# Kernel tuning notes

Hardware: AMD Instinct MI355X
Metric: run time of the kernel (lower is better)

The kernel has to match this reference:

```python
import jax, jax.numpy as jnp
import numpy as np

N, D = 8192, 4096

def setup_inputs() -> dict:
    key = jax.random.key(0)
    k1, k2 = jax.random.split(key)
    # inputs = [mean | var]; shift uniform by +0.1 so var > 0 (log + division)
    inputs = jax.random.uniform(k1, (N, 2 * D), dtype=jnp.float32) + 0.1
    targets = jax.random.normal(k2, (N, D), dtype=jnp.float32)
    return {"inputs": inputs, "targets": targets}

def reference(inputs, targets):
    size = targets.shape[1]
    mean = inputs[:, :size]          # [N, D]
    var = inputs[:, size:]           # [N, D]
    diff = mean - targets            # [N, D]
    mid = diff / var                 # [N, D]
    lg = jnp.log(jnp.sum(var))
    # Faithful to the torch code: full DxD gram matrix, then its trace.
    out = jnp.trace(jnp.matmul(diff.T, mid)) + lg
    return out
```

## Files before the change

kernel.cpp:

```cpp
#include <hip/hip_runtime.h>


constexpr int N = 8192;
constexpr int D = 4096;
constexpr int BLOCKS = 2048;
constexpr int THREADS = 256;

__global__ __launch_bounds__(THREADS) void loss_partial_kernel(
    const float* __restrict__ inputs,
    const float* __restrict__ targets,
    float* __restrict__ partials)
{
    const long long total4  = (long long)N * D / 4;
    const long long nthread = (long long)gridDim.x * blockDim.x;

    float s1 = 0.0f;
    float s2 = 0.0f;

    long long i = (long long)blockIdx.x * blockDim.x + threadIdx.x;
    #pragma unroll 4
    for (int it = 0; it < 16; ++it, i += nthread) {
        const long long row  = i >> 10;
        const long long col4 = (i & 1023) << 2;

        const float4 m = *(const float4*)(inputs  + row * (2LL * D) + col4);
        const float4 v = *(const float4*)(inputs  + row * (2LL * D) + D + col4);
        const float4 t = *(const float4*)(targets + (i << 2));

        const float d0 = m.x - t.x;
        const float d1 = m.y - t.y;
        const float d2 = m.z - t.z;
        const float d3 = m.w - t.w;

        s1 += d0 * d0 * __builtin_amdgcn_rcpf(v.x);
        s1 += d1 * d1 * __builtin_amdgcn_rcpf(v.y);
        s1 += d2 * d2 * __builtin_amdgcn_rcpf(v.z);
        s1 += d3 * d3 * __builtin_amdgcn_rcpf(v.w);
        s2 += (v.x + v.y) + (v.z + v.w);
    }

    #pragma unroll
    for (int off = 32; off > 0; off >>= 1) {
        s1 += __shfl_down(s1, off, 64);
        s2 += __shfl_down(s2, off, 64);
    }

    __shared__ float l1[THREADS / 64];
    __shared__ float l2[THREADS / 64];
    const int wave = threadIdx.x >> 6;
    const int lane = threadIdx.x & 63;
    if (lane == 0) { l1[wave] = s1; l2[wave] = s2; }
    __syncthreads();

    if (threadIdx.x == 0) {
        float a = l1[0] + l1[1] + l1[2] + l1[3];
        float b = l2[0] + l2[1] + l2[2] + l2[3];
        partials[blockIdx.x]          = a;
        partials[BLOCKS + blockIdx.x] = b;
    }
}

__global__ __launch_bounds__(256) void loss_final_kernel(
    const float* __restrict__ partials,
    float* __restrict__ out)
{
    double s1 = 0.0, s2 = 0.0;
    for (int i = threadIdx.x; i < BLOCKS; i += 256) {
        s1 += (double)partials[i];
        s2 += (double)partials[BLOCKS + i];
    }

    #pragma unroll
    for (int off = 32; off > 0; off >>= 1) {
        s1 += __shfl_down(s1, off, 64);
        s2 += __shfl_down(s2, off, 64);
    }

    __shared__ double l1[4];
    __shared__ double l2[4];
    const int wave = threadIdx.x >> 6;
    const int lane = threadIdx.x & 63;
    if (lane == 0) { l1[wave] = s1; l2[wave] = s2; }
    __syncthreads();

    if (threadIdx.x == 0) {
        const double a = l1[0] + l1[1] + l1[2] + l1[3];
        const double b = l2[0] + l2[1] + l2[2] + l2[3];
        out[0] = (float)(a + log(b));
    }
}

extern "C" void kernel_launch(void* const* d_in, const int* in_sizes, int n_in,
                              void* d_out, int out_size, void* d_ws, size_t ws_size,
                              hipStream_t stream) {
    const float* inputs  = (const float*)d_in[0];
    const float* targets = (const float*)d_in[1];
    float* out      = (float*)d_out;
    float* partials = (float*)d_ws;

    loss_partial_kernel<<<BLOCKS, THREADS, 0, stream>>>(inputs, targets, partials);
    loss_final_kernel<<<1, 256, 0, stream>>>(partials, out);
}
```

Measured before the change: 80.15 us.

## Fuse final reduction into main kernel via atomics and last-block finalize

Drops the separate finalize kernel. Each block now atomically adds its partial sums into a workspace, and the last block (found with an atomic counter) writes the loss. The streaming loads switch to nontemporal loads with 32-bit index math and a smaller unroll, and the launch bounds gain an occupancy hint. In exchange a memset launch is added, and the float atomic accumulation is non-deterministic and less precise than the earlier double reduction.

New measurement: 262.8 us. 228% more time.

```diff
diff --git a/kernel.cpp b/kernel.cpp
--- a/kernel.cpp
+++ b/kernel.cpp
@@ -1,4 +1,5 @@
 #include <hip/hip_runtime.h>
+#include <math.h>
 
 
 constexpr int N = 8192;
@@ -6,26 +7,31 @@
 constexpr int BLOCKS = 2048;
 constexpr int THREADS = 256;
 
-__global__ __launch_bounds__(THREADS) void loss_partial_kernel(
+typedef float f32x4 __attribute__((ext_vector_type(4)));
+
+__global__ __launch_bounds__(THREADS, 8) void loss_fused_kernel(
     const float* __restrict__ inputs,
     const float* __restrict__ targets,
-    float* __restrict__ partials)
+    float* __restrict__ ws,
+    float* __restrict__ out)
 {
-    const long long total4  = (long long)N * D / 4;
-    const long long nthread = (long long)gridDim.x * blockDim.x;
+    constexpr unsigned NTHREAD = (unsigned)BLOCKS * THREADS;
 
     float s1 = 0.0f;
     float s2 = 0.0f;
 
-    long long i = (long long)blockIdx.x * blockDim.x + threadIdx.x;
-    #pragma unroll 4
-    for (int it = 0; it < 16; ++it, i += nthread) {
-        const long long row  = i >> 10;
-        const long long col4 = (i & 1023) << 2;
+    unsigned i = blockIdx.x * (unsigned)THREADS + threadIdx.x;
+    #pragma unroll 2
+    for (int it = 0; it < 16; ++it, i += NTHREAD) {
+        const unsigned row  = i >> 10;
+        const unsigned col4 = (i & 1023u) << 2;
 
-        const float4 m = *(const float4*)(inputs  + row * (2LL * D) + col4);
-        const float4 v = *(const float4*)(inputs  + row * (2LL * D) + D + col4);
-        const float4 t = *(const float4*)(targets + (i << 2));
+        const f32x4 m = __builtin_nontemporal_load(
+            (const f32x4*)(inputs + (size_t)row * 8192u + col4));
+        const f32x4 v = __builtin_nontemporal_load(
+            (const f32x4*)(inputs + (size_t)row * 8192u + 4096u + col4));
+        const f32x4 t = __builtin_nontemporal_load(
+            (const f32x4*)(targets + (size_t)i * 4u));
 
         const float d0 = m.x - t.x;
         const float d1 = m.y - t.y;
@@ -53,40 +59,20 @@
     __syncthreads();
 
     if (threadIdx.x == 0) {
-        float a = l1[0] + l1[1] + l1[2] + l1[3];
-        float b = l2[0] + l2[1] + l2[2] + l2[3];
-        partials[blockIdx.x]          = a;
-        partials[BLOCKS + blockIdx.x] = b;
-    }
-}
-
-__global__ __launch_bounds__(256) void loss_final_kernel(
-    const float* __restrict__ partials,
-    float* __restrict__ out)
-{
-    double s1 = 0.0, s2 = 0.0;
-    for (int i = threadIdx.x; i < BLOCKS; i += 256) {
-        s1 += (double)partials[i];
-        s2 += (double)partials[BLOCKS + i];
-    }
-
-    #pragma unroll
-    for (int off = 32; off > 0; off >>= 1) {
-        s1 += __shfl_down(s1, off, 64);
-        s2 += __shfl_down(s2, off, 64);
-    }
-
-    __shared__ double l1[4];
-    __shared__ double l2[4];
-    const int wave = threadIdx.x >> 6;
-    const int lane = threadIdx.x & 63;
-    if (lane == 0) { l1[wave] = s1; l2[wave] = s2; }
-    __syncthreads();
-
-    if (threadIdx.x == 0) {
-        const double a = l1[0] + l1[1] + l1[2] + l1[3];
-        const double b = l2[0] + l2[1] + l2[2] + l2[3];
-        out[0] = (float)(a + log(b));
+        const float a = (l1[0] + l1[1]) + (l1[2] + l1[3]);
+        const float b = (l2[0] + l2[1]) + (l2[2] + l2[3]);
+        atomicAdd(&ws[0], a);
+        atomicAdd(&ws[1], b);
+        __threadfence();
+        const unsigned old = __hip_atomic_fetch_add(
+            (unsigned*)&ws[3], 1u, __ATOMIC_ACQ_REL, __HIP_MEMORY_SCOPE_AGENT);
+        if (old == (unsigned)BLOCKS - 1u) {
+            const float fs1 = __hip_atomic_load(&ws[0], __ATOMIC_RELAXED,
+                                                __HIP_MEMORY_SCOPE_AGENT);
+            const float fs2 = __hip_atomic_load(&ws[1], __ATOMIC_RELAXED,
+                                                __HIP_MEMORY_SCOPE_AGENT);
+            out[0] = fs1 + logf(fs2);
+        }
     }
 }
 
@@ -95,9 +81,9 @@
                               hipStream_t stream) {
     const float* inputs  = (const float*)d_in[0];
     const float* targets = (const float*)d_in[1];
-    float* out      = (float*)d_out;
-    float* partials = (float*)d_ws;
+    float* out = (float*)d_out;
+    float* ws  = (float*)d_ws;
 
-    loss_partial_kernel<<<BLOCKS, THREADS, 0, stream>>>(inputs, targets, partials);
-    loss_final_kernel<<<1, 256, 0, stream>>>(partials, out);
+    (void)hipMemsetAsync(ws, 0, 16, stream);
+    loss_fused_kernel<<<BLOCKS, THREADS, 0, stream>>>(inputs, targets, ws, out);
 }
```
